# Kernel optimization log

Hardware: AMD Instinct MI355X
Metric: run time of the kernel (lower is better)

## Reference

```python
import jax, jax.numpy as jnp
import numpy as np
from jax.scipy.ndimage import map_coordinates


def setup_inputs() -> dict:
    key = jax.random.key(0)
    k1, k2 = jax.random.split(key)
    B, C, H, W = 8, 4, 1024, 1024
    image = jax.random.normal(k1, (B, C, H, W), dtype=jnp.float32)
    # flow in pixels; scale a bit so displacements span several pixels
    flow = jax.random.normal(k2, (B, 2, H, W), dtype=jnp.float32) * 4.0
    return {"image": image, "flow": flow}


def _warp(image, flow):
    # image: [B, C, H, W], flow: [B, 2, H, W] (x-disp at channel 0, y-disp at channel 1)
    B, C, H, W = image.shape
    dt = flow.dtype
    xx = jnp.arange(W, dtype=dt)[None, None, :]   # [1,1,W]
    yy = jnp.arange(H, dtype=dt)[None, :, None]   # [1,H,1]
    vx = xx + flow[:, 0]                           # [B,H,W] absolute x coordinate
    vy = yy + flow[:, 1]                           # [B,H,W] absolute y coordinate
    # Source normalizes with the align_corners=True formula...
    gx = 2.0 * vx / max(W - 1, 1) - 1.0
    gy = 2.0 * vy / max(H - 1, 1) - 1.0
    # ...but samples with align_corners=False: unnormalize accordingly.
    ix = ((gx + 1.0) * W - 1.0) * 0.5
    iy = ((gy + 1.0) * H - 1.0) * 0.5
    # padding_mode='border': clamp source coordinates into the valid range.
    ix = jnp.clip(ix, 0.0, W - 1)
    iy = jnp.clip(iy, 0.0, H - 1)

    def sample_plane(img2d, iy_b, ix_b):
        # bilinear gather; mode='nearest' clamps indices (matches border padding)
        return map_coordinates(img2d, [iy_b, ix_b], order=1, mode='nearest')

    # vmap over batch, then over channels (coords shared across channels)
    per_batch = lambda img, iy_b, ix_b: jax.vmap(lambda c: sample_plane(c, iy_b, ix_b))(img)
    return jax.vmap(per_batch)(image, iy, ix)  # [B,C,H,W]


def reference(image, flow):
    return _warp(image, flow)
```

## Files before the change

### kernel.cpp

```cpp
#include <hip/hip_runtime.h>


#define BB 8
#define CC 4
#define HH 1024
#define WW 1024
#define HW (HH * WW)

#define TX 64
#define TY 16
#define HALO 16
#define RW 98
#define RH 49
#define NENT (RH * (RW / 2))

typedef _Float16 h4 __attribute__((ext_vector_type(4)));
typedef _Float16 h8 __attribute__((ext_vector_type(8)));

__global__ __launch_bounds__(512, 8) void advect_fused_kernel(
    const float* __restrict__ image,
    const float* __restrict__ flow,
    float* __restrict__ out)
{
    __shared__ h4 lds[RH][RW];

    const int tid = threadIdx.x;
    const int x0 = blockIdx.x * TX;
    const int y0 = blockIdx.y * TY;
    const int b  = blockIdx.z;

    const float* img = image + (size_t)b * CC * HW;

#pragma unroll
    for (int i = 0; i < 5; ++i) {
        const int e = i * 512 + tid;
        if (e < NENT) {
            const int r  = e / (RW / 2);
            const int pc = e - r * (RW / 2);
            const int gy  = min(max(y0 - HALO + r, 0), HH - 1);
            const int gxb = min(max(x0 - HALO + 2 * pc, 0), WW - 2);
            const float* p = img + (size_t)gy * WW + gxb;
            float2 c0, c1, c2, c3;
            __builtin_memcpy(&c0, p,          8);
            __builtin_memcpy(&c1, p + HW,     8);
            __builtin_memcpy(&c2, p + 2 * HW, 8);
            __builtin_memcpy(&c3, p + 3 * HW, 8);
            h8 pr;
            pr[0] = (_Float16)c0.x; pr[1] = (_Float16)c1.x;
            pr[2] = (_Float16)c2.x; pr[3] = (_Float16)c3.x;
            pr[4] = (_Float16)c0.y; pr[5] = (_Float16)c1.y;
            pr[6] = (_Float16)c2.y; pr[7] = (_Float16)c3.y;
            *(h8*)&lds[r][2 * pc] = pr;
        }
    }
    __syncthreads();

    const int tx  = tid & 63;
    const int x   = x0 + tx;
    const int ty0 = tid >> 6;

    const float sxs = (float)WW / (float)(WW - 1);
    const float sys = (float)HH / (float)(HH - 1);

    const float* flb = flow + (size_t)b * 2 * HW;
    float* outb = out + (size_t)b * CC * HW;

#pragma unroll
    for (int k = 0; k < 2; ++k) {
        const int y = y0 + ty0 + (k << 3);
        const float* fl = flb + (size_t)y * WW + x;
        const float fx = __builtin_nontemporal_load(fl);
        const float fy = __builtin_nontemporal_load(fl + HW);

        float ix = ((float)x + fx) * sxs - 0.5f;
        float iy = ((float)y + fy) * sys - 0.5f;
        ix = fminf(fmaxf(ix, 0.0f), (float)(WW - 1));
        iy = fminf(fmaxf(iy, 0.0f), (float)(HH - 1));
        const int xl = min((int)ix, WW - 2);
        const int yl = min((int)iy, HH - 2);
        const float wx = ix - (float)xl;
        const float wy = iy - (float)yl;
        const float u0 = 1.0f - wx;
        const float v0 = 1.0f - wy;

        const int rx = xl - x0 + HALO;
        const int ry = yl - y0 + HALO;

        float o0, o1, o2, o3;
        if ((unsigned)rx <= (unsigned)(RW - 2) && (unsigned)ry <= (unsigned)(RH - 2)) {
            const h4 a00 = lds[ry][rx];
            const h4 a01 = lds[ry][rx + 1];
            const h4 a10 = lds[ry + 1][rx];
            const h4 a11 = lds[ry + 1][rx + 1];
            o0 = v0 * (u0 * (float)a00[0] + wx * (float)a01[0])
               + wy * (u0 * (float)a10[0] + wx * (float)a11[0]);
            o1 = v0 * (u0 * (float)a00[1] + wx * (float)a01[1])
               + wy * (u0 * (float)a10[1] + wx * (float)a11[1]);
            o2 = v0 * (u0 * (float)a00[2] + wx * (float)a01[2])
               + wy * (u0 * (float)a10[2] + wx * (float)a11[2]);
            o3 = v0 * (u0 * (float)a00[3] + wx * (float)a01[3])
               + wy * (u0 * (float)a10[3] + wx * (float)a11[3]);
        } else {
            const size_t o00 = (size_t)yl * WW + xl;
            float2 t, bt;
            const float* p0 = img + o00;
            __builtin_memcpy(&t,  p0,      8);
            __builtin_memcpy(&bt, p0 + WW, 8);
            o0 = v0 * (u0 * t.x + wx * t.y) + wy * (u0 * bt.x + wx * bt.y);
            p0 += HW;
            __builtin_memcpy(&t,  p0,      8);
            __builtin_memcpy(&bt, p0 + WW, 8);
            o1 = v0 * (u0 * t.x + wx * t.y) + wy * (u0 * bt.x + wx * bt.y);
            p0 += HW;
            __builtin_memcpy(&t,  p0,      8);
            __builtin_memcpy(&bt, p0 + WW, 8);
            o2 = v0 * (u0 * t.x + wx * t.y) + wy * (u0 * bt.x + wx * bt.y);
            p0 += HW;
            __builtin_memcpy(&t,  p0,      8);
            __builtin_memcpy(&bt, p0 + WW, 8);
            o3 = v0 * (u0 * t.x + wx * t.y) + wy * (u0 * bt.x + wx * bt.y);
        }

        const size_t op = (size_t)y * WW + x;
        __builtin_nontemporal_store(o0, &outb[op]);
        __builtin_nontemporal_store(o1, &outb[HW + op]);
        __builtin_nontemporal_store(o2, &outb[2 * (size_t)HW + op]);
        __builtin_nontemporal_store(o3, &outb[3 * (size_t)HW + op]);
    }
}

extern "C" void kernel_launch(void* const* d_in, const int* in_sizes, int n_in,
                              void* d_out, int out_size, void* d_ws, size_t ws_size,
                              hipStream_t stream) {
    const float* image = (const float*)d_in[0];
    const float* flow  = (const float*)d_in[1];
    float* out = (float*)d_out;

    dim3 grid(WW / TX, HH / TY, BB);
    advect_fused_kernel<<<grid, 512, 0, stream>>>(image, flow, out);
}
```

Baseline: 292.9 us.

## Enlarge tile to 64x32, shrink halo, float4 staging loads, prefetch flow before sync

The tile height doubles to 32 rows and the halo shrinks to 12/11 pixels, so each block stages a smaller fraction of redundant halo data into LDS per output pixel. The LDS fill now uses float4 global loads and writes two h8 entries per thread. All four rows of flow values are loaded before the staging loop so their latency overlaps the image fill and the barrier. The smaller halo sends more samples with large displacements to the slow global-memory fallback path. The extra prefetched registers could also lower occupancy.

```diff
diff --git a/kernel.cpp b/kernel.cpp
--- a/kernel.cpp
+++ b/kernel.cpp
@@ -8,11 +8,13 @@
 #define HW (HH * WW)
 
 #define TX 64
-#define TY 16
-#define HALO 16
-#define RW 98
-#define RH 49
-#define NENT (RH * (RW / 2))
+#define TY 32
+#define HXL 12
+#define HYT 11
+#define RW 88
+#define RH 56
+#define NQ (RW / 4)
+#define NENT (RH * NQ)
 
 typedef _Float16 h4 __attribute__((ext_vector_type(4)));
 typedef _Float16 h8 __attribute__((ext_vector_type(8)));
@@ -30,47 +32,58 @@
     const int b  = blockIdx.z;
 
     const float* img = image + (size_t)b * CC * HW;
-
-#pragma unroll
-    for (int i = 0; i < 5; ++i) {
-        const int e = i * 512 + tid;
-        if (e < NENT) {
-            const int r  = e / (RW / 2);
-            const int pc = e - r * (RW / 2);
-            const int gy  = min(max(y0 - HALO + r, 0), HH - 1);
-            const int gxb = min(max(x0 - HALO + 2 * pc, 0), WW - 2);
-            const float* p = img + (size_t)gy * WW + gxb;
-            float2 c0, c1, c2, c3;
-            __builtin_memcpy(&c0, p,          8);
-            __builtin_memcpy(&c1, p + HW,     8);
-            __builtin_memcpy(&c2, p + 2 * HW, 8);
-            __builtin_memcpy(&c3, p + 3 * HW, 8);
-            h8 pr;
-            pr[0] = (_Float16)c0.x; pr[1] = (_Float16)c1.x;
-            pr[2] = (_Float16)c2.x; pr[3] = (_Float16)c3.x;
-            pr[4] = (_Float16)c0.y; pr[5] = (_Float16)c1.y;
-            pr[6] = (_Float16)c2.y; pr[7] = (_Float16)c3.y;
-            *(h8*)&lds[r][2 * pc] = pr;
-        }
-    }
-    __syncthreads();
+    const float* flb = flow + (size_t)b * 2 * HW;
 
     const int tx  = tid & 63;
     const int x   = x0 + tx;
     const int ty0 = tid >> 6;
 
+    float pfx[4], pfy[4];
+#pragma unroll
+    for (int k = 0; k < 4; ++k) {
+        const float* fl = flb + (size_t)(y0 + ty0 + (k << 3)) * WW + x;
+        pfx[k] = __builtin_nontemporal_load(fl);
+        pfy[k] = __builtin_nontemporal_load(fl + HW);
+    }
+
+#pragma unroll
+    for (int i = 0; i < 3; ++i) {
+        const int e = i * 512 + tid;
+        if (e < NENT) {
+            const int r = e / NQ;
+            const int q = e - r * NQ;
+            const int gy = min(max(y0 - HYT + r, 0), HH - 1);
+            const int gx = min(max(x0 - HXL + 4 * q, 0), WW - 4);
+            const float* p = img + (size_t)gy * WW + gx;
+            const float4 c0 = *reinterpret_cast<const float4*>(p);
+            const float4 c1 = *reinterpret_cast<const float4*>(p + HW);
+            const float4 c2 = *reinterpret_cast<const float4*>(p + 2 * HW);
+            const float4 c3 = *reinterpret_cast<const float4*>(p + 3 * HW);
+            h8 lo, hi;
+            lo[0] = (_Float16)c0.x; lo[1] = (_Float16)c1.x;
+            lo[2] = (_Float16)c2.x; lo[3] = (_Float16)c3.x;
+            lo[4] = (_Float16)c0.y; lo[5] = (_Float16)c1.y;
+            lo[6] = (_Float16)c2.y; lo[7] = (_Float16)c3.y;
+            hi[0] = (_Float16)c0.z; hi[1] = (_Float16)c1.z;
+            hi[2] = (_Float16)c2.z; hi[3] = (_Float16)c3.z;
+            hi[4] = (_Float16)c0.w; hi[5] = (_Float16)c1.w;
+            hi[6] = (_Float16)c2.w; hi[7] = (_Float16)c3.w;
+            *(h8*)&lds[r][4 * q]     = lo;
+            *(h8*)&lds[r][4 * q + 2] = hi;
+        }
+    }
+    __syncthreads();
+
     const float sxs = (float)WW / (float)(WW - 1);
     const float sys = (float)HH / (float)(HH - 1);
 
-    const float* flb = flow + (size_t)b * 2 * HW;
     float* outb = out + (size_t)b * CC * HW;
 
 #pragma unroll
-    for (int k = 0; k < 2; ++k) {
+    for (int k = 0; k < 4; ++k) {
         const int y = y0 + ty0 + (k << 3);
-        const float* fl = flb + (size_t)y * WW + x;
-        const float fx = __builtin_nontemporal_load(fl);
-        const float fy = __builtin_nontemporal_load(fl + HW);
+        const float fx = pfx[k];
+        const float fy = pfy[k];
 
         float ix = ((float)x + fx) * sxs - 0.5f;
         float iy = ((float)y + fy) * sys - 0.5f;
@@ -83,8 +96,8 @@
         const float u0 = 1.0f - wx;
         const float v0 = 1.0f - wy;
 
-        const int rx = xl - x0 + HALO;
-        const int ry = yl - y0 + HALO;
+        const int rx = xl - x0 + HXL;
+        const int ry = yl - y0 + HYT;
 
         float o0, o1, o2, o3;
         if ((unsigned)rx <= (unsigned)(RW - 2) && (unsigned)ry <= (unsigned)(RH - 2)) {
```

After: 273.3 us. 1.07x faster.
